# Kernel tuning notes

Measured on AMD Instinct MI355X. Metric: run time of the kernel, lower is better.

Reference implementation:

```python
import jax, jax.numpy as jnp
import numpy as np

SLOT_DIM = 256
HIDDEN = 128
NUM_REL = 8


def setup_inputs() -> dict:
    key = jax.random.key(0)
    ks = jax.random.split(key, 5)
    B, N, D = 8, 256, SLOT_DIM
    slots = jax.random.normal(ks[0], (B, N, D), dtype=jnp.float32)
    # Linear(2D -> H): store as [2D, H] (x @ W + b)
    s1 = 1.0 / np.sqrt(2 * D)
    W1 = jax.random.uniform(ks[1], (2 * D, HIDDEN), jnp.float32, -s1, s1)
    b1 = jax.random.uniform(ks[2], (HIDDEN,), jnp.float32, -s1, s1)
    s2 = 1.0 / np.sqrt(HIDDEN)
    W2 = jax.random.uniform(ks[3], (HIDDEN, NUM_REL), jnp.float32, -s2, s2)
    b2 = jax.random.uniform(ks[4], (NUM_REL,), jnp.float32, -s2, s2)
    return {"slots": slots, "W1": W1, "b1": b1, "W2": W2, "b2": b2}


def reference(slots, W1, b1, W2, b2):
    # cat([slots_i, slots_j]) @ W1 == slots_i @ W1[:D] + slots_j @ W1[D:]
    # so project each slot once, then broadcast-add over the pair grid.
    D = slots.shape[-1]
    proj_i = jnp.einsum("bnd,dh->bnh", slots, W1[:D])   # [B,N,H]
    proj_j = jnp.einsum("bnd,dh->bnh", slots, W1[D:])   # [B,N,H]
    h = proj_i[:, :, None, :] + proj_j[:, None, :, :] + b1  # [B,N,N,H]
    h = jax.nn.relu(h)
    logits = jnp.einsum("bijh,hr->bijr", h, W2) + b2     # [B,N,N,R]
    return jax.nn.sigmoid(logits)
```

## Files before the change

### kernel.cpp

```cpp
#include <hip/hip_runtime.h>
#include <hip/hip_fp16.h>
#include <math.h>

#define BATCH 8
#define NSLOT 256
#define DDIM  256
#define HID   128
#define NREL  8

typedef _Float16 half8 __attribute__((ext_vector_type(8)));
typedef float float4v __attribute__((ext_vector_type(4)));

union U8 {
  uint32_t u[4];
  _Float16 f[8];
  half8 v;
  float4 f4;
};


__global__ __launch_bounds__(256) void proj_kernel(
    const float* __restrict__ slots, const float* __restrict__ W1,
    const float* __restrict__ b1, _Float16* __restrict__ P) {
  const int lane = threadIdx.x & 63;
  const int w    = threadIdx.x >> 6;
  const int lo16 = lane & 15;
  const int kg   = lane >> 4;
  const int row0 = blockIdx.y * 16;
  const int c    = (blockIdx.x * 4 + w) * 16 + lo16;

  const float* Wcol =
      (c < HID) ? (W1 + c) : (W1 + (size_t)DDIM * HID + (c - HID));
  U8 bf[8];
#pragma unroll
  for (int ks = 0; ks < 8; ++ks) {
    const int kb = ks * 32 + kg * 8;
#pragma unroll
    for (int u = 0; u < 8; ++u)
      bf[ks].f[u] = (_Float16)Wcol[(size_t)(kb + u) * HID];
  }

  float4v acc = {0.0f, 0.0f, 0.0f, 0.0f};
  const float* srow = slots + (size_t)(row0 + lo16) * DDIM;
#pragma unroll
  for (int ks = 0; ks < 8; ++ks) {
    const float4 x0 = *(const float4*)(srow + ks * 32 + kg * 8);
    const float4 x1 = *(const float4*)(srow + ks * 32 + kg * 8 + 4);
    U8 a;
    a.f[0] = (_Float16)x0.x; a.f[1] = (_Float16)x0.y;
    a.f[2] = (_Float16)x0.z; a.f[3] = (_Float16)x0.w;
    a.f[4] = (_Float16)x1.x; a.f[5] = (_Float16)x1.y;
    a.f[6] = (_Float16)x1.z; a.f[7] = (_Float16)x1.w;
    acc = __builtin_amdgcn_mfma_f32_16x16x32_f16(a.v, bf[ks].v, acc, 0, 0, 0);
  }

  const float bias = (c < HID) ? b1[c] : 0.0f;
#pragma unroll
  for (int reg = 0; reg < 4; ++reg)
    P[(size_t)(row0 + kg * 4 + reg) * 256 + c] = (_Float16)(acc[reg] + bias);
}

__global__ __launch_bounds__(256) void pair_kernel(
    const _Float16* __restrict__ P, const float* __restrict__ W2,
    const float* __restrict__ b2, float* __restrict__ out) {
  __shared__ uint32_t PiL[8 * 68];

  const int tid  = threadIdx.x;
  const int w    = tid >> 6;
  const int lane = tid & 63;
  const int n    = lane & 15;
  const int kg   = lane >> 4;

  const int b  = blockIdx.z;
  const int i0 = blockIdx.y * 8;
  const int j0 = blockIdx.x * 64 + w * 16;
  const _Float16* Pb = P + (size_t)b * NSLOT * 256;

  if (tid < 128) {
    const int r  = tid >> 4;
    const int ch = tid & 15;
    const float4 t = *(const float4*)(Pb + (size_t)(i0 + r) * 256 + ch * 8);
    *(float4*)&PiL[r * 68 + ch * 4] = t;
  }

  U8 w2f[4];
#pragma unroll
  for (int kq = 0; kq < 4; ++kq) {
    const int kb = kq * 32 + kg * 8;
#pragma unroll
    for (int u = 0; u < 8; ++u) {
      const float v = W2[(kb + u) * NREL + (n & 7)];
      w2f[kq].f[u] = (n < NREL) ? (_Float16)v : (_Float16)0.0f;
    }
  }

  const float b2v = (n < NREL) ? b2[n & 7] : 0.0f;

  U8 pj[4];
#pragma unroll
  for (int kq = 0; kq < 4; ++kq)
    pj[kq].f4 =
        *(const float4*)(Pb + (size_t)(j0 + n) * 256 + HID + kq * 32 + kg * 8);

  __syncthreads();

#pragma unroll
  for (int i = 0; i < 8; ++i) {
    float4v acc = {0.0f, 0.0f, 0.0f, 0.0f};
#pragma unroll
    for (int kq = 0; kq < 4; ++kq) {
      U8 pi;
      pi.f4 = *(const float4*)&PiL[i * 68 + kq * 16 + kg * 4];
      U8 h;
      h.v = __builtin_elementwise_max(pj[kq].v + pi.v, (half8)(_Float16)0.0f);
      acc = __builtin_amdgcn_mfma_f32_16x16x32_f16(h.v, w2f[kq].v, acc, 0, 0, 0);
    }
    if (n < NREL) {
      float* obase =
          out + (((size_t)b * NSLOT + (i0 + i)) * NSLOT + j0) * NREL + n;
#pragma unroll
      for (int reg = 0; reg < 4; ++reg) {
        const int jrow = kg * 4 + reg;
        const float x = acc[reg] + b2v;
        obase[jrow * NREL] = __builtin_amdgcn_rcpf(1.0f + __expf(-x));
      }
    }
  }
}

extern "C" void kernel_launch(void* const* d_in, const int* in_sizes, int n_in,
                              void* d_out, int out_size, void* d_ws,
                              size_t ws_size, hipStream_t stream) {
  const float* slots = (const float*)d_in[0];
  const float* W1    = (const float*)d_in[1];
  const float* b1    = (const float*)d_in[2];
  const float* W2    = (const float*)d_in[3];
  const float* b2    = (const float*)d_in[4];
  float* out  = (float*)d_out;
  _Float16* P = (_Float16*)d_ws;

  proj_kernel<<<dim3(4, 128), 256, 0, stream>>>(slots, W1, b1, P);
  pair_kernel<<<dim3(NSLOT / 64, NSLOT / 8, BATCH), 256, 0, stream>>>(P, W2,
                                                                      b2, out);
}
```

Before: 79.65 us.

## Fuse projection and pair kernels into one cooperative kernel with grid sync

```diff
diff --git a/kernel.cpp b/kernel.cpp
--- a/kernel.cpp
+++ b/kernel.cpp
@@ -1,6 +1,9 @@
 #include <hip/hip_runtime.h>
+#include <hip/hip_cooperative_groups.h>
 #include <hip/hip_fp16.h>
 #include <math.h>
+
+namespace cg = cooperative_groups;
 
 #define BATCH 8
 #define NSLOT 256
@@ -18,111 +21,119 @@
   float4 f4;
 };
 
-
-__global__ __launch_bounds__(256) void proj_kernel(
+__global__ __launch_bounds__(256, 4) void fused_kernel(
     const float* __restrict__ slots, const float* __restrict__ W1,
-    const float* __restrict__ b1, _Float16* __restrict__ P) {
-  const int lane = threadIdx.x & 63;
-  const int w    = threadIdx.x >> 6;
-  const int lo16 = lane & 15;
-  const int kg   = lane >> 4;
-  const int row0 = blockIdx.y * 16;
-  const int c    = (blockIdx.x * 4 + w) * 16 + lo16;
-
-  const float* Wcol =
-      (c < HID) ? (W1 + c) : (W1 + (size_t)DDIM * HID + (c - HID));
-  U8 bf[8];
-#pragma unroll
-  for (int ks = 0; ks < 8; ++ks) {
-    const int kb = ks * 32 + kg * 8;
-#pragma unroll
-    for (int u = 0; u < 8; ++u)
-      bf[ks].f[u] = (_Float16)Wcol[(size_t)(kb + u) * HID];
-  }
-
-  float4v acc = {0.0f, 0.0f, 0.0f, 0.0f};
-  const float* srow = slots + (size_t)(row0 + lo16) * DDIM;
-#pragma unroll
-  for (int ks = 0; ks < 8; ++ks) {
-    const float4 x0 = *(const float4*)(srow + ks * 32 + kg * 8);
-    const float4 x1 = *(const float4*)(srow + ks * 32 + kg * 8 + 4);
-    U8 a;
-    a.f[0] = (_Float16)x0.x; a.f[1] = (_Float16)x0.y;
-    a.f[2] = (_Float16)x0.z; a.f[3] = (_Float16)x0.w;
-    a.f[4] = (_Float16)x1.x; a.f[5] = (_Float16)x1.y;
-    a.f[6] = (_Float16)x1.z; a.f[7] = (_Float16)x1.w;
-    acc = __builtin_amdgcn_mfma_f32_16x16x32_f16(a.v, bf[ks].v, acc, 0, 0, 0);
-  }
-
-  const float bias = (c < HID) ? b1[c] : 0.0f;
-#pragma unroll
-  for (int reg = 0; reg < 4; ++reg)
-    P[(size_t)(row0 + kg * 4 + reg) * 256 + c] = (_Float16)(acc[reg] + bias);
-}
-
-__global__ __launch_bounds__(256) void pair_kernel(
-    const _Float16* __restrict__ P, const float* __restrict__ W2,
-    const float* __restrict__ b2, float* __restrict__ out) {
+    const float* __restrict__ b1, const float* __restrict__ W2,
+    const float* __restrict__ b2, float* __restrict__ out,
+    _Float16* __restrict__ P) {
   __shared__ uint32_t PiL[8 * 68];
 
   const int tid  = threadIdx.x;
   const int w    = tid >> 6;
   const int lane = tid & 63;
-  const int n    = lane & 15;
+  const int lo16 = lane & 15;
   const int kg   = lane >> 4;
 
-  const int b  = blockIdx.z;
-  const int i0 = blockIdx.y * 8;
-  const int j0 = blockIdx.x * 64 + w * 16;
-  const _Float16* Pb = P + (size_t)b * NSLOT * 256;
+  {
+    const int t = blockIdx.x * 4 + w;
+    if (t < 2048) {
+      const int ct   = t & 15;
+      const int rb   = t >> 4;
+      const int row0 = rb * 16;
+      const int c    = ct * 16 + lo16;
 
-  if (tid < 128) {
-    const int r  = tid >> 4;
-    const int ch = tid & 15;
-    const float4 t = *(const float4*)(Pb + (size_t)(i0 + r) * 256 + ch * 8);
-    *(float4*)&PiL[r * 68 + ch * 4] = t;
-  }
+      const float* Wcol =
+          (c < HID) ? (W1 + c) : (W1 + (size_t)DDIM * HID + (c - HID));
+      U8 bf[8];
+#pragma unroll
+      for (int ks = 0; ks < 8; ++ks) {
+        const int kb = ks * 32 + kg * 8;
+#pragma unroll
+        for (int u = 0; u < 8; ++u)
+          bf[ks].f[u] = (_Float16)Wcol[(size_t)(kb + u) * HID];
+      }
 
-  U8 w2f[4];
+      float4v acc = {0.0f, 0.0f, 0.0f, 0.0f};
+      const float* srow = slots + (size_t)(row0 + lo16) * DDIM;
 #pragma unroll
-  for (int kq = 0; kq < 4; ++kq) {
-    const int kb = kq * 32 + kg * 8;
+      for (int ks = 0; ks < 8; ++ks) {
+        const float4 x0 = *(const float4*)(srow + ks * 32 + kg * 8);
+        const float4 x1 = *(const float4*)(srow + ks * 32 + kg * 8 + 4);
+        U8 a;
+        a.f[0] = (_Float16)x0.x; a.f[1] = (_Float16)x0.y;
+        a.f[2] = (_Float16)x0.z; a.f[3] = (_Float16)x0.w;
+        a.f[4] = (_Float16)x1.x; a.f[5] = (_Float16)x1.y;
+        a.f[6] = (_Float16)x1.z; a.f[7] = (_Float16)x1.w;
+        acc =
+            __builtin_amdgcn_mfma_f32_16x16x32_f16(a.v, bf[ks].v, acc, 0, 0, 0);
+      }
+
+      const float bias = (c < HID) ? b1[c] : 0.0f;
 #pragma unroll
-    for (int u = 0; u < 8; ++u) {
-      const float v = W2[(kb + u) * NREL + (n & 7)];
-      w2f[kq].f[u] = (n < NREL) ? (_Float16)v : (_Float16)0.0f;
+      for (int reg = 0; reg < 4; ++reg)
+        P[(size_t)(row0 + kg * 4 + reg) * 256 + c] = (_Float16)(acc[reg] + bias);
     }
   }
 
-  const float b2v = (n < NREL) ? b2[n & 7] : 0.0f;
+  cg::this_grid().sync();
 
-  U8 pj[4];
+  {
+    const int bx = blockIdx.x;
+    const int b  = bx >> 7;
+    const int i0 = ((bx >> 2) & 31) * 8;
+    const int j0 = (bx & 3) * 64 + w * 16;
+    const int n  = lo16;
+    const _Float16* Pb = P + (size_t)b * NSLOT * 256;
+
+    if (tid < 128) {
+      const int r  = tid >> 4;
+      const int ch = tid & 15;
+      const float4 t = *(const float4*)(Pb + (size_t)(i0 + r) * 256 + ch * 8);
+      *(float4*)&PiL[r * 68 + ch * 4] = t;
+    }
+
+    U8 w2f[4];
 #pragma unroll
-  for (int kq = 0; kq < 4; ++kq)
-    pj[kq].f4 =
-        *(const float4*)(Pb + (size_t)(j0 + n) * 256 + HID + kq * 32 + kg * 8);
+    for (int kq = 0; kq < 4; ++kq) {
+      const int kb = kq * 32 + kg * 8;
+#pragma unroll
+      for (int u = 0; u < 8; ++u) {
+        const float v = W2[(kb + u) * NREL + (n & 7)];
+        w2f[kq].f[u] = (n < NREL) ? (_Float16)v : (_Float16)0.0f;
+      }
+    }
 
-  __syncthreads();
+    const float b2v = (n < NREL) ? b2[n & 7] : 0.0f;
+
+    U8 pj[4];
+#pragma unroll
+    for (int kq = 0; kq < 4; ++kq)
+      pj[kq].f4 = *(const float4*)(Pb + (size_t)(j0 + n) * 256 + HID +
+                                   kq * 32 + kg * 8);
+
+    __syncthreads();
 
 #pragma unroll
-  for (int i = 0; i < 8; ++i) {
-    float4v acc = {0.0f, 0.0f, 0.0f, 0.0f};
+    for (int i = 0; i < 8; ++i) {
+      float4v acc = {0.0f, 0.0f, 0.0f, 0.0f};
 #pragma unroll
-    for (int kq = 0; kq < 4; ++kq) {
-      U8 pi;
-      pi.f4 = *(const float4*)&PiL[i * 68 + kq * 16 + kg * 4];
-      U8 h;
-      h.v = __builtin_elementwise_max(pj[kq].v + pi.v, (half8)(_Float16)0.0f);
-      acc = __builtin_amdgcn_mfma_f32_16x16x32_f16(h.v, w2f[kq].v, acc, 0, 0, 0);
-    }
-    if (n < NREL) {
-      float* obase =
-          out + (((size_t)b * NSLOT + (i0 + i)) * NSLOT + j0) * NREL + n;
+      for (int kq = 0; kq < 4; ++kq) {
+        U8 pi;
+        pi.f4 = *(const float4*)&PiL[i * 68 + kq * 16 + kg * 4];
+        U8 h;
+        h.v = __builtin_elementwise_max(pj[kq].v + pi.v, (half8)(_Float16)0.0f);
+        acc =
+            __builtin_amdgcn_mfma_f32_16x16x32_f16(h.v, w2f[kq].v, acc, 0, 0, 0);
+      }
+      if (n < NREL) {
+        float* obase =
+            out + (((size_t)b * NSLOT + (i0 + i)) * NSLOT + j0) * NREL + n;
 #pragma unroll
-      for (int reg = 0; reg < 4; ++reg) {
-        const int jrow = kg * 4 + reg;
-        const float x = acc[reg] + b2v;
-        obase[jrow * NREL] = __builtin_amdgcn_rcpf(1.0f + __expf(-x));
+        for (int reg = 0; reg < 4; ++reg) {
+          const int jrow = kg * 4 + reg;
+          const float x = acc[reg] + b2v;
+          obase[jrow * NREL] = __builtin_amdgcn_rcpf(1.0f + __expf(-x));
+        }
       }
     }
   }
@@ -139,7 +150,8 @@
   float* out  = (float*)d_out;
   _Float16* P = (_Float16*)d_ws;
 
-  proj_kernel<<<dim3(4, 128), 256, 0, stream>>>(slots, W1, b1, P);
-  pair_kernel<<<dim3(NSLOT / 64, NSLOT / 8, BATCH), 256, 0, stream>>>(P, W2,
-                                                                      b2, out);
+  void* args[] = {(void*)&slots, (void*)&W1, (void*)&b1, (void*)&W2,
+                  (void*)&b2,    (void*)&out, (void*)&P};
+  hipLaunchCooperativeKernel((const void*)fused_kernel, dim3(1024), dim3(256),
+                             args, 0, stream);
 }
```

Result: slower. 196.5 us (+146.6%).

## Fuse projection and pair kernels, recomputing j-projection per block in LDS

Applied to the files above, without the earlier changes.

```diff
diff --git a/kernel.cpp b/kernel.cpp
--- a/kernel.cpp
+++ b/kernel.cpp
@@ -18,111 +18,177 @@
   float4 f4;
 };
 
-
-__global__ __launch_bounds__(256) void proj_kernel(
+union U4 {
+  uint32_t u[2];
+  _Float16 f[4];
+  uint2 u2;
+};
+
+
+__device__ __forceinline__ int swz(int row, int off) {
+  return (off & ~0x70) | ((((off >> 4) ^ row) & 7) << 4);
+}
+
+__global__ __launch_bounds__(512, 2) void fused_kernel(
     const float* __restrict__ slots, const float* __restrict__ W1,
-    const float* __restrict__ b1, _Float16* __restrict__ P) {
-  const int lane = threadIdx.x & 63;
-  const int w    = threadIdx.x >> 6;
-  const int lo16 = lane & 15;
-  const int kg   = lane >> 4;
-  const int row0 = blockIdx.y * 16;
-  const int c    = (blockIdx.x * 4 + w) * 16 + lo16;
-
-  const float* Wcol =
-      (c < HID) ? (W1 + c) : (W1 + (size_t)DDIM * HID + (c - HID));
-  U8 bf[8];
-#pragma unroll
-  for (int ks = 0; ks < 8; ++ks) {
-    const int kb = ks * 32 + kg * 8;
-#pragma unroll
-    for (int u = 0; u < 8; ++u)
-      bf[ks].f[u] = (_Float16)Wcol[(size_t)(kb + u) * HID];
-  }
-
-  float4v acc = {0.0f, 0.0f, 0.0f, 0.0f};
-  const float* srow = slots + (size_t)(row0 + lo16) * DDIM;
-#pragma unroll
-  for (int ks = 0; ks < 8; ++ks) {
-    const float4 x0 = *(const float4*)(srow + ks * 32 + kg * 8);
-    const float4 x1 = *(const float4*)(srow + ks * 32 + kg * 8 + 4);
-    U8 a;
-    a.f[0] = (_Float16)x0.x; a.f[1] = (_Float16)x0.y;
-    a.f[2] = (_Float16)x0.z; a.f[3] = (_Float16)x0.w;
-    a.f[4] = (_Float16)x1.x; a.f[5] = (_Float16)x1.y;
-    a.f[6] = (_Float16)x1.z; a.f[7] = (_Float16)x1.w;
-    acc = __builtin_amdgcn_mfma_f32_16x16x32_f16(a.v, bf[ks].v, acc, 0, 0, 0);
-  }
-
-  const float bias = (c < HID) ? b1[c] : 0.0f;
-#pragma unroll
-  for (int reg = 0; reg < 4; ++reg)
-    P[(size_t)(row0 + kg * 4 + reg) * 256 + c] = (_Float16)(acc[reg] + bias);
-}
-
-__global__ __launch_bounds__(256) void pair_kernel(
-    const _Float16* __restrict__ P, const float* __restrict__ W2,
+    const float* __restrict__ b1, const float* __restrict__ W2,
     const float* __restrict__ b2, float* __restrict__ out) {
-  __shared__ uint32_t PiL[8 * 68];
+  __shared__ _Float16 WuS[128 * 256];
+  __shared__ _Float16 SlabS[8][2][16 * 128];
+  __shared__ _Float16 PiS[8 * 128];
 
   const int tid  = threadIdx.x;
   const int w    = tid >> 6;
   const int lane = tid & 63;
-  const int n    = lane & 15;
+  const int lo16 = lane & 15;
   const int kg   = lane >> 4;
 
-  const int b  = blockIdx.z;
-  const int i0 = blockIdx.y * 8;
-  const int j0 = blockIdx.x * 64 + w * 16;
-  const _Float16* Pb = P + (size_t)b * NSLOT * 256;
-
-  if (tid < 128) {
-    const int r  = tid >> 4;
-    const int ch = tid & 15;
-    const float4 t = *(const float4*)(Pb + (size_t)(i0 + r) * 256 + ch * 8);
-    *(float4*)&PiL[r * 68 + ch * 4] = t;
-  }
-
+  const int b  = blockIdx.y;
+  const int i0 = blockIdx.x * 8;
+  const float* sb = slots + (size_t)b * NSLOT * DDIM;
+
+  {
+    const int c = tid & 127;
+    const int kb0 = tid >> 7;
+    const float* Wup = W1 + (size_t)DDIM * HID;
+#pragma unroll
+    for (int s = 0; s < 8; ++s) {
+      const int kb = kb0 + s * 4;
+      U8 p;
+#pragma unroll
+      for (int u = 0; u < 8; ++u)
+        p.f[u] = (_Float16)Wup[(size_t)(kb * 8 + u) * HID + c];
+      *(float4*)((char*)WuS + c * 512 + swz(c, kb * 16)) = p.f4;
+    }
+  }
+
+  {
+    const int c = w * 16 + lo16;
+    const float* Wcol = W1 + c;
+    U8 bf[8];
+#pragma unroll
+    for (int ks = 0; ks < 8; ++ks) {
+      const int kb = ks * 32 + kg * 8;
+#pragma unroll
+      for (int u = 0; u < 8; ++u)
+        bf[ks].f[u] = (_Float16)Wcol[(size_t)(kb + u) * HID];
+    }
+    int arow = i0 + lo16;
+    if (arow > NSLOT - 1) arow = NSLOT - 1;
+    const float* srow = sb + (size_t)arow * DDIM;
+    float4v acc = {0.0f, 0.0f, 0.0f, 0.0f};
+#pragma unroll
+    for (int ks = 0; ks < 8; ++ks) {
+      const float4 x0 = *(const float4*)(srow + ks * 32 + kg * 8);
+      const float4 x1 = *(const float4*)(srow + ks * 32 + kg * 8 + 4);
+      U8 a;
+      a.f[0] = (_Float16)x0.x; a.f[1] = (_Float16)x0.y;
+      a.f[2] = (_Float16)x0.z; a.f[3] = (_Float16)x0.w;
+      a.f[4] = (_Float16)x1.x; a.f[5] = (_Float16)x1.y;
+      a.f[6] = (_Float16)x1.z; a.f[7] = (_Float16)x1.w;
+      acc = __builtin_amdgcn_mfma_f32_16x16x32_f16(a.v, bf[ks].v, acc, 0, 0, 0);
+    }
+    const float bias = b1[c];
+#pragma unroll
+    for (int reg = 0; reg < 4; ++reg) {
+      const int m = kg * 4 + reg;
+      if (m < 8) PiS[m * 128 + c] = (_Float16)(acc[reg] + bias);
+    }
+  }
+
+  U8 Bs[2][8];
+#pragma unroll
+  for (int t = 0; t < 2; ++t) {
+    const int j0t = (2 * w + t) * 16;
+    const float* srow = sb + (size_t)(j0t + lo16) * DDIM;
+#pragma unroll
+    for (int ks = 0; ks < 8; ++ks) {
+      const float4 x0 = *(const float4*)(srow + ks * 32 + kg * 8);
+      const float4 x1 = *(const float4*)(srow + ks * 32 + kg * 8 + 4);
+      Bs[t][ks].f[0] = (_Float16)x0.x; Bs[t][ks].f[1] = (_Float16)x0.y;
+      Bs[t][ks].f[2] = (_Float16)x0.z; Bs[t][ks].f[3] = (_Float16)x0.w;
+      Bs[t][ks].f[4] = (_Float16)x1.x; Bs[t][ks].f[5] = (_Float16)x1.y;
+      Bs[t][ks].f[6] = (_Float16)x1.z; Bs[t][ks].f[7] = (_Float16)x1.w;
+    }
+  }
   U8 w2f[4];
 #pragma unroll
   for (int kq = 0; kq < 4; ++kq) {
     const int kb = kq * 32 + kg * 8;
 #pragma unroll
     for (int u = 0; u < 8; ++u) {
-      const float v = W2[(kb + u) * NREL + (n & 7)];
-      w2f[kq].f[u] = (n < NREL) ? (_Float16)v : (_Float16)0.0f;
-    }
-  }
-
-  const float b2v = (n < NREL) ? b2[n & 7] : 0.0f;
-
-  U8 pj[4];
-#pragma unroll
-  for (int kq = 0; kq < 4; ++kq)
-    pj[kq].f4 =
-        *(const float4*)(Pb + (size_t)(j0 + n) * 256 + HID + kq * 32 + kg * 8);
+      const float v = W2[(kb + u) * NREL + (lo16 & 7)];
+      w2f[kq].f[u] = (lo16 < NREL) ? (_Float16)v : (_Float16)0.0f;
+    }
+  }
+  const float b2v = (lo16 < NREL) ? b2[lo16 & 7] : 0.0f;
 
   __syncthreads();
 
+  _Float16* myslab0 = &SlabS[w][0][0];
+  _Float16* myslab1 = &SlabS[w][1][0];
+#pragma unroll
+  for (int ct = 0; ct < 8; ++ct) {
+    const int c = ct * 16 + lo16;
+    U8 af[8];
+#pragma unroll
+    for (int ks = 0; ks < 8; ++ks)
+      af[ks].f4 = *(const float4*)((const char*)WuS + c * 512 +
+                                   swz(c, ks * 64 + kg * 16));
+    float4v d0 = {0.0f, 0.0f, 0.0f, 0.0f};
+    float4v d1 = {0.0f, 0.0f, 0.0f, 0.0f};
+#pragma unroll
+    for (int ks = 0; ks < 8; ++ks) {
+      d0 = __builtin_amdgcn_mfma_f32_16x16x32_f16(af[ks].v, Bs[0][ks].v, d0, 0, 0, 0);
+      d1 = __builtin_amdgcn_mfma_f32_16x16x32_f16(af[ks].v, Bs[1][ks].v, d1, 0, 0, 0);
+    }
+    U4 s0, s1;
+#pragma unroll
+    for (int r4 = 0; r4 < 4; ++r4) {
+      s0.f[r4] = (_Float16)d0[r4];
+      s1.f[r4] = (_Float16)d1[r4];
+    }
+    const int off = ct * 32 + kg * 8;
+    *(uint2*)((char*)myslab0 + lo16 * 256 + swz(lo16, off)) = s0.u2;
+    *(uint2*)((char*)myslab1 + lo16 * 256 + swz(lo16, off)) = s1.u2;
+  }
+
+  U8 pjf[2][4];
+#pragma unroll
+  for (int t = 0; t < 2; ++t) {
+    const char* base = (const char*)(t ? myslab1 : myslab0);
+#pragma unroll
+    for (int kq = 0; kq < 4; ++kq)
+      pjf[t][kq].f4 = *(const float4*)(base + lo16 * 256 +
+                                       swz(lo16, kq * 64 + kg * 16));
+  }
+
 #pragma unroll
   for (int i = 0; i < 8; ++i) {
-    float4v acc = {0.0f, 0.0f, 0.0f, 0.0f};
-#pragma unroll
-    for (int kq = 0; kq < 4; ++kq) {
-      U8 pi;
-      pi.f4 = *(const float4*)&PiL[i * 68 + kq * 16 + kg * 4];
-      U8 h;
-      h.v = __builtin_elementwise_max(pj[kq].v + pi.v, (half8)(_Float16)0.0f);
-      acc = __builtin_amdgcn_mfma_f32_16x16x32_f16(h.v, w2f[kq].v, acc, 0, 0, 0);
-    }
-    if (n < NREL) {
-      float* obase =
-          out + (((size_t)b * NSLOT + (i0 + i)) * NSLOT + j0) * NREL + n;
-#pragma unroll
-      for (int reg = 0; reg < 4; ++reg) {
-        const int jrow = kg * 4 + reg;
-        const float x = acc[reg] + b2v;
-        obase[jrow * NREL] = __builtin_amdgcn_rcpf(1.0f + __expf(-x));
+    U8 pif[4];
+#pragma unroll
+    for (int kq = 0; kq < 4; ++kq)
+      pif[kq].f4 = *(const float4*)&PiS[i * 128 + kq * 32 + kg * 8];
+#pragma unroll
+    for (int t = 0; t < 2; ++t) {
+      const int j0t = (2 * w + t) * 16;
+      float4v acc = {0.0f, 0.0f, 0.0f, 0.0f};
+#pragma unroll
+      for (int kq = 0; kq < 4; ++kq) {
+        U8 h;
+        h.v = __builtin_elementwise_max(pjf[t][kq].v + pif[kq].v,
+                                        (half8)(_Float16)0.0f);
+        acc = __builtin_amdgcn_mfma_f32_16x16x32_f16(h.v, w2f[kq].v, acc, 0, 0, 0);
+      }
+      if (lo16 < NREL) {
+        float* obase =
+            out + (((size_t)b * NSLOT + (i0 + i)) * NSLOT + j0t) * NREL + lo16;
+#pragma unroll
+        for (int reg = 0; reg < 4; ++reg) {
+          const int jrow = kg * 4 + reg;
+          const float x = acc[reg] + b2v;
+          obase[jrow * NREL] = __builtin_amdgcn_rcpf(1.0f + __expf(-x));
+        }
       }
     }
   }
@@ -136,10 +202,9 @@
   const float* b1    = (const float*)d_in[2];
   const float* W2    = (const float*)d_in[3];
   const float* b2    = (const float*)d_in[4];
-  float* out  = (float*)d_out;
-  _Float16* P = (_Float16*)d_ws;
-
-  proj_kernel<<<dim3(4, 128), 256, 0, stream>>>(slots, W1, b1, P);
-  pair_kernel<<<dim3(NSLOT / 64, NSLOT / 8, BATCH), 256, 0, stream>>>(P, W2,
-                                                                      b2, out);
+  float* out = (float*)d_out;
+  (void)d_ws; (void)ws_size;
+
+  fused_kernel<<<dim3(NSLOT / 8, BATCH), 512, 0, stream>>>(slots, W1, b1, W2,
+                                                           b2, out);
 }
```

After: 87.36 us. 9.7% more time.
